# Kernel optimization log

Hardware: AMD Instinct MI355X
Metric: run time of the kernel (lower is better)

Reference implementation:

```python
import jax, jax.numpy as jnp
import numpy as np

N, E, IN, H, OUT, G = 100000, 1600000, 9, 64, 6, 1024
EPS = 1e-5


def setup_inputs() -> dict:
    key = jax.random.key(0)
    ks = jax.random.split(key, 24)
    inp = {
        "x": jax.random.normal(ks[0], (N, IN), dtype=jnp.float32),
        "edge_index": jax.random.randint(ks[1], (2, E), 0, N, dtype=jnp.int64),
        "edge_weight": jax.random.uniform(ks[2], (E,), dtype=jnp.float32),
        "batch": jnp.sort(jax.random.randint(ks[3], (N,), 0, G, dtype=jnp.int64)),
    }
    def lin(k, fan_in, fan_out):
        return jax.random.normal(k, (fan_in, fan_out), dtype=jnp.float32) / np.sqrt(fan_in)
    # GraphConv layer 0: IN -> H; layers 1,2: H -> H
    inp["W_rel0"], inp["W_root0"], inp["b0"] = lin(ks[4], IN, H), lin(ks[5], IN, H), jnp.zeros((H,), jnp.float32)
    inp["W_rel1"], inp["W_root1"], inp["b1"] = lin(ks[6], H, H), lin(ks[7], H, H), jnp.zeros((H,), jnp.float32)
    inp["W_rel2"], inp["W_root2"], inp["b2"] = lin(ks[8], H, H), lin(ks[9], H, H), jnp.zeros((H,), jnp.float32)
    # BatchNorm params for the first num_layers-1 = 2 layers
    inp["g0"], inp["be0"] = jnp.ones((H,), jnp.float32), jnp.zeros((H,), jnp.float32)
    inp["g1"], inp["be1"] = jnp.ones((H,), jnp.float32), jnp.zeros((H,), jnp.float32)
    # MLP head
    inp["W_l1"], inp["b_l1"] = lin(ks[10], H, H), jnp.zeros((H,), jnp.float32)
    inp["W_l2"], inp["b_l2"] = lin(ks[11], H, OUT), jnp.zeros((OUT,), jnp.float32)
    return inp


def graph_conv(x, src, dst, ew, W_rel, W_root, b):
    # PyG GraphConv: out = aggr_add(e_ji * x_j) @ W_rel + b + x @ W_root
    msg = x[src] * ew[:, None]                      # [E, F] gather
    agg = jax.ops.segment_sum(msg, dst, num_segments=x.shape[0])  # [N, F] scatter-add
    return agg @ W_rel + b + x @ W_root


def batch_norm(x, g, b):
    m = jnp.mean(x, axis=0)
    v = jnp.var(x, axis=0)
    return (x - m) * jax.lax.rsqrt(v + EPS) * g + b


def reference(x, edge_index, edge_weight, batch,
              W_rel0, W_root0, b0, W_rel1, W_root1, b1, W_rel2, W_root2, b2,
              g0, be0, g1, be1, W_l1, b_l1, W_l2, b_l2):
    src, dst = edge_index[0], edge_index[1]
    # layer 0: conv -> BN -> relu (dropout p applied only in training; eval here)
    h = graph_conv(x, src, dst, edge_weight, W_rel0, W_root0, b0)
    h = jax.nn.relu(batch_norm(h, g0, be0))
    # layer 1
    h = graph_conv(h, src, dst, edge_weight, W_rel1, W_root1, b1)
    h = jax.nn.relu(batch_norm(h, g1, be1))
    # layer 2 (no norm/relu)
    h = graph_conv(h, src, dst, edge_weight, W_rel2, W_root2, b2)
    # global mean pool over graphs
    summed = jax.ops.segment_sum(h, batch, num_segments=G)            # [G, H]
    counts = jax.ops.segment_sum(jnp.ones((h.shape[0],), h.dtype), batch, num_segments=G)
    pooled = summed / jnp.maximum(counts, 1.0)[:, None]
    # MLP head
    z = jax.nn.relu(pooled @ W_l1 + b_l1)
    return z @ W_l2 + b_l2
```

## Files before the change

kernel.cpp:

```cpp
#include <hip/hip_runtime.h>
#include <hip/hip_fp16.h>

constexpr int N    = 100000;
constexpr int E    = 1600000;
constexpr int FIN  = 9;
constexpr int OUTF = 6;
constexpr int G    = 1024;
constexpr int NPB  = 256;
constexpr int NB   = (N + NPB - 1) / NPB;
constexpr int CH   = 2048;
constexpr int NCH  = (E + CH - 1) / CH;
constexpr int BCAP = 4864;
constexpr int CBCAP= BCAP + NPB + 8;
constexpr int EBUF = 5888;
constexpr int ZCNT = 256 + G * 64;

typedef _Float16 f16x8 __attribute__((ext_vector_type(8)));
typedef float    f32x4 __attribute__((ext_vector_type(4)));

__device__ __forceinline__ void atomAddF(float* p, float v) { unsafeAtomicAdd(p, v); }

__global__ __launch_bounds__(256) void initK(int* __restrict__ cursor, float* __restrict__ zeros,
    const float* __restrict__ x, __half* __restrict__ x9)
{
    int i = blockIdx.x * 256 + threadIdx.x;
    if (i < NB) cursor[i] = i * BCAP;
    if (i < ZCNT) zeros[i] = 0.f;
    if (i < N * FIN) x9[i] = __float2half(x[i]);
}

__global__ __launch_bounds__(256) void passA(const int* __restrict__ src, const int* __restrict__ dst,
    const float* __restrict__ ew, int* __restrict__ cursor, int2* __restrict__ bucketed)
{
    __shared__ int h[NB];
    __shared__ int hb[NB];
    int t = threadIdx.x;
    for (int i = t; i < NB; i += 256) h[i] = 0;
    __syncthreads();
    int base = blockIdx.x * CH;
    int myS[8], myD[8], rk[8]; float myW[8];
#pragma unroll
    for (int i = 0; i < 8; i++) {
        int e = base + i * 256 + t;
        if (e < E) {
            myS[i] = src[e]; myD[i] = dst[e]; myW[i] = ew[e];
            rk[i] = atomicAdd(&h[myD[i] >> 8], 1);
        } else myD[i] = -1;
    }
    __syncthreads();
    for (int i = t; i < NB; i += 256) hb[i] = h[i] ? atomicAdd(&cursor[i], h[i]) : 0;
    __syncthreads();
#pragma unroll
    for (int i = 0; i < 8; i++) if (myD[i] >= 0) {
        int packed = myS[i] | ((myD[i] & 255) << 24);
        bucketed[hb[myD[i] >> 8] + rk[i]] = make_int2(packed, __float_as_int(myW[i]));
    }
}

__global__ __launch_bounds__(NPB) void passB(const int* __restrict__ cursor,
    const int2* __restrict__ bucketed, int* __restrict__ ebeg, int* __restrict__ eend,
    int2* __restrict__ csr)
{
    __shared__ int2 ebuf[EBUF];
    __shared__ int cl[NPB], sa[NPB], sb[NPB], curs[NPB];
    int b = blockIdx.x, t = threadIdx.x;
    int node0 = b * NPB;
    int nnode = min(NPB, N - node0);
    int cnt = cursor[b] - b * BCAP;
    int abase = b * BCAP;
    int base = b * CBCAP;
    bool fits = (cnt <= EBUF);
    cl[t] = 0;
    __syncthreads();
    for (int e = t; e < cnt; e += NPB) {
        int2 r = bucketed[abase + e];
        if (fits) ebuf[e] = r;
        atomicAdd(&cl[((unsigned)r.x) >> 24], 1);
    }
    __syncthreads();
    int deg = cl[t];
    int pc = (deg + 1) & ~1;
    int* cur = sa; int* nxt = sb;
    cur[t] = pc;
    __syncthreads();
    for (int o = 1; o < NPB; o <<= 1) {
        int v = cur[t];
        if (t >= o) v += cur[t - o];
        nxt[t] = v;
        __syncthreads();
        int* tmp = cur; cur = nxt; nxt = tmp;
    }
    int off = cur[t] - pc;
    if (t < nnode) { ebeg[node0 + t] = base + off; eend[node0 + t] = base + off + deg; }
    curs[t] = off;
    __syncthreads();
    for (int e = t; e < cnt; e += NPB) {
        int2 r = fits ? ebuf[e] : bucketed[abase + e];
        int dl = ((unsigned)r.x) >> 24;
        int pos = base + atomicAdd(&curs[dl], 1);
        csr[pos] = make_int2(r.x & 0x00FFFFFF, r.y);
    }
    __syncthreads();
    if (t < nnode && (deg & 1)) csr[base + off + deg] = make_int2(0, 0);
    if (t < 4) csr[base + cur[NPB - 1] + t] = make_int2(0, 0);
}

__global__ __launch_bounds__(256) void wprep(const float* __restrict__ Wrel1, const float* __restrict__ Wroot1,
    const float* __restrict__ Wrel2, const float* __restrict__ Wroot2, __half* __restrict__ Wt)
{
    int i = blockIdx.x * 256 + threadIdx.x;
    int layer = i >> 13, r = i & 8191;
    int c = r >> 6, k = r & 63;
    const float* Wrel = layer ? Wrel2 : Wrel1;
    const float* Wroot = layer ? Wroot2 : Wroot1;
    float v = (c < 64) ? Wrel[k * 64 + c] : Wroot[k * 64 + (c - 64)];
    Wt[i] = __float2half(v);
}

__global__ __launch_bounds__(256) void gather9(const __half* __restrict__ x9,
    const int2* __restrict__ csr, const int* __restrict__ ebeg, const int* __restrict__ eend,
    float* __restrict__ agg9)
{
    int t = threadIdx.x, lane = t & 63;
    int es = lane >> 4, fc = min(lane & 15, FIN - 1);
    int wv = (blockIdx.x * blockDim.x + t) >> 6;
    int nw = (gridDim.x * blockDim.x) >> 6;
    for (int n = wv; n < N; n += nw) {
        int beg = ebeg[n], end = eend[n];
        int last = end - 1;
        int2 eA0 = csr[min(beg + es,      last)];
        int2 eB0 = csr[min(beg + 4 + es,  last)];
        int2 eA1 = csr[min(beg + 8 + es,  last)];
        int2 eB1 = csr[min(beg + 12 + es, last)];
        __half xA = x9[(size_t)eA0.x * FIN + fc];
        __half xB = x9[(size_t)eB0.x * FIN + fc];
        float a0 = 0.f, a1 = 0.f;
        for (int k = beg; k < end; k += 8) {
            int2 eA2 = csr[min(k + 16 + es, last)];
            int2 eB2 = csr[min(k + 20 + es, last)];
            __half nxA = x9[(size_t)eA1.x * FIN + fc];
            __half nxB = x9[(size_t)eB1.x * FIN + fc];
            float wA = (k + es     < end) ? __int_as_float(eA0.y) : 0.f;
            float wB = (k + 4 + es < end) ? __int_as_float(eB0.y) : 0.f;
            a0 = fmaf(wA, __half2float(xA), a0);
            a1 = fmaf(wB, __half2float(xB), a1);
            eA0 = eA1; eB0 = eB1; eA1 = eA2; eB1 = eB2;
            xA = nxA; xB = nxB;
        }
        float r = a0 + a1;
        r += __shfl(r, lane ^ 16, 64);
        r += __shfl(r, lane ^ 32, 64);
        if (lane < FIN) agg9[(size_t)n * FIN + lane] = r;
    }
}

__global__ __launch_bounds__(256) void proj0post(const float* __restrict__ x,
    const float* __restrict__ agg9, const float* __restrict__ Wrel,
    const float* __restrict__ Wroot, const float* __restrict__ bias,
    __half* __restrict__ H0, float* __restrict__ stats)
{
    int t = threadIdx.x, j = t & 63;
    int nl = __builtin_amdgcn_readfirstlane(t >> 6);
    float wrel[FIN], wroot[FIN];
#pragma unroll
    for (int k = 0; k < FIN; k++) { wrel[k] = Wrel[k * 64 + j]; wroot[k] = Wroot[k * 64 + j]; }
    float bj = bias[j];
    float s1 = 0.f, s2 = 0.f;
    const int ntiles = N / 4;
    for (int tile = blockIdx.x; tile < ntiles; tile += gridDim.x) {
        int n = tile * 4 + nl;
        const float* xr = x + (size_t)n * FIN;
        const float* ar = agg9 + (size_t)n * FIN;
        float acc = bj;
#pragma unroll
        for (int k = 0; k < FIN; k++) {
            acc = fmaf(ar[k], wrel[k], acc);
            acc = fmaf(xr[k], wroot[k], acc);
        }
        H0[(size_t)n * 64 + j] = __float2half(acc);
        s1 += acc; s2 += acc * acc;
    }
    __shared__ float sred[256];
    sred[t] = s1; __syncthreads();
    if (t < 64) atomAddF(&stats[t], sred[t] + sred[t+64] + sred[t+128] + sred[t+192]);
    __syncthreads();
    sred[t] = s2; __syncthreads();
    if (t < 64) atomAddF(&stats[64 + t], sred[t] + sred[t+64] + sred[t+128] + sred[t+192]);
}

__global__ __launch_bounds__(256) void projm(const __half* __restrict__ Hin, const __half* __restrict__ Wt,
    const float* __restrict__ bias, const float* __restrict__ stats,
    const float* __restrict__ gam, const float* __restrict__ bet,
    __half* __restrict__ P, __half* __restrict__ Hout)
{
    int t = threadIdx.x, lane = t & 63;
    int wv = blockIdx.x * 4 + (t >> 6);
    int nw = gridDim.x * 4;
    int n16 = lane & 15, quad = lane >> 4;
    constexpr float invN = 1.0f / (float)N;
    float sc[16], sh[16];
#pragma unroll
    for (int jj = 0; jj < 16; jj++) {
        int k = (jj < 8) ? (quad * 8 + jj) : (32 + quad * 8 + (jj - 8));
        float m = stats[k] * invN;
        float v = stats[64 + k] * invN - m * m;
        sc[jj] = gam[k] * rsqrtf(v + 1e-5f);
        sh[jj] = bet[k] - m * sc[jj];
    }
    f16x8 bf[8][2];
#pragma unroll
    for (int ct = 0; ct < 8; ct++)
#pragma unroll
        for (int kh = 0; kh < 2; kh++)
            bf[ct][kh] = *(const f16x8*)(Wt + (size_t)(ct * 16 + n16) * 64 + kh * 32 + quad * 8);
    float bcol[4];
#pragma unroll
    for (int i = 0; i < 4; i++) bcol[i] = bias[i * 16 + n16];
    const int NT = N / 16;
    for (int tile = wv; tile < NT; tile += nw) {
        int n0 = tile * 16;
        f16x8 r0 = *(const f16x8*)(Hin + (size_t)(n0 + n16) * 64 + quad * 8);
        f16x8 r1 = *(const f16x8*)(Hin + (size_t)(n0 + n16) * 64 + 32 + quad * 8);
        f16x8 a0, a1;
#pragma unroll
        for (int jj = 0; jj < 8; jj++) {
            a0[jj] = (_Float16)fmaxf(fmaf((float)r0[jj], sc[jj],     sh[jj]),     0.f);
            a1[jj] = (_Float16)fmaxf(fmaf((float)r1[jj], sc[jj + 8], sh[jj + 8]), 0.f);
        }
        f32x4 acc[8];
#pragma unroll
        for (int ct = 0; ct < 8; ct++) {
            f32x4 c = {0.f, 0.f, 0.f, 0.f};
            c = __builtin_amdgcn_mfma_f32_16x16x32_f16(a0, bf[ct][0], c, 0, 0, 0);
            c = __builtin_amdgcn_mfma_f32_16x16x32_f16(a1, bf[ct][1], c, 0, 0, 0);
            acc[ct] = c;
        }
#pragma unroll
        for (int ct = 0; ct < 8; ct++) {
#pragma unroll
            for (int r = 0; r < 4; r++) {
                int n = n0 + quad * 4 + r;
                if (ct < 4) P[(size_t)n * 64 + ct * 16 + n16] = __float2half(acc[ct][r]);
                else Hout[(size_t)n * 64 + (ct - 4) * 16 + n16] = __float2half(acc[ct][r] + bcol[ct - 4]);
            }
        }
    }
}

template<int EPI>
__global__ __launch_bounds__(256) void gather(const __half* __restrict__ P, __half* H,
    const int2* __restrict__ csr, const int* __restrict__ ebeg, const int* __restrict__ eend,
    float* __restrict__ stats, const int* __restrict__ batch, float* __restrict__ pool)
{
    int t = threadIdx.x, lane = t & 63;
    int wv = (blockIdx.x * blockDim.x + t) >> 6;
    int nw = (gridDim.x * blockDim.x) >> 6;
    float s1 = 0.f, s2 = 0.f;
    const int NPAIR = N / 2;
    for (int pr = wv; pr < NPAIR; pr += nw) {
        int n0 = 2 * pr, n1 = n0 + 1;
        int b0 = ebeg[n0], m0 = (eend[n0] - b0 + 1) >> 1;
        int b1 = ebeg[n1], m1 = (eend[n1] - b1 + 1) >> 1;
        const int4* q0 = (const int4*)csr + (b0 >> 1);
        const int4* q1 = (const int4*)csr + (b1 >> 1);
        int c0 = max(m0 - 1, 0), c1 = max(m1 - 1, 0);
        float x0 = __half2float(H[(size_t)n0 * 64 + lane]);
        float x1 = __half2float(H[(size_t)n1 * 64 + lane]);
        int4 qaA = q0[0],           qbA = q0[min(1, c0)];
        int4 qcA = q1[0],           qdA = q1[min(1, c1)];
        int4 qaB = q0[min(2, c0)],  qbB = q0[min(3, c0)];
        int4 qcB = q1[min(2, c1)],  qdB = q1[min(3, c1)];
        __half pa0 = P[(size_t)qaA.x * 64 + lane], pa1 = P[(size_t)qaA.z * 64 + lane];
        __half pb0 = P[(size_t)qbA.x * 64 + lane], pb1 = P[(size_t)qbA.z * 64 + lane];
        __half pc0 = P[(size_t)qcA.x * 64 + lane], pc1 = P[(size_t)qcA.z * 64 + lane];
        __half pd0 = P[(size_t)qdA.x * 64 + lane], pd1 = P[(size_t)qdA.z * 64 + lane];
        float a0 = 0.f, a1 = 0.f, a2 = 0.f, a3 = 0.f;
        float a4 = 0.f, a5 = 0.f, a6 = 0.f, a7 = 0.f;
        int mm = max(m0, m1);
        for (int k = 0; k < mm; k += 2) {
            int4 qaC = q0[min(k + 4, c0)], qbC = q0[min(k + 5, c0)];
            int4 qcC = q1[min(k + 4, c1)], qdC = q1[min(k + 5, c1)];
            __half na0 = P[(size_t)qaB.x * 64 + lane], na1 = P[(size_t)qaB.z * 64 + lane];
            __half nb0 = P[(size_t)qbB.x * 64 + lane], nb1 = P[(size_t)qbB.z * 64 + lane];
            __half nc0 = P[(size_t)qcB.x * 64 + lane], nc1 = P[(size_t)qcB.z * 64 + lane];
            __half nd0 = P[(size_t)qdB.x * 64 + lane], nd1 = P[(size_t)qdB.z * 64 + lane];
            float wa = (k     < m0) ? __int_as_float(qaA.y) : 0.f;
            float wA = (k     < m0) ? __int_as_float(qaA.w) : 0.f;
            float wb = (k + 1 < m0) ? __int_as_float(qbA.y) : 0.f;
            float wB = (k + 1 < m0) ? __int_as_float(qbA.w) : 0.f;
            float wc = (k     < m1) ? __int_as_float(qcA.y) : 0.f;
            float wC = (k     < m1) ? __int_as_float(qcA.w) : 0.f;
            float wd = (k + 1 < m1) ? __int_as_float(qdA.y) : 0.f;
            float wD = (k + 1 < m1) ? __int_as_float(qdA.w) : 0.f;
            a0 = fmaf(wa, __half2float(pa0), a0); a1 = fmaf(wA, __half2float(pa1), a1);
            a2 = fmaf(wb, __half2float(pb0), a2); a3 = fmaf(wB, __half2float(pb1), a3);
            a4 = fmaf(wc, __half2float(pc0), a4); a5 = fmaf(wC, __half2float(pc1), a5);
            a6 = fmaf(wd, __half2float(pd0), a6); a7 = fmaf(wD, __half2float(pd1), a7);
            qaA = qaB; qbA = qbB; qcA = qcB; qdA = qdB;
            qaB = qaC; qbB = qbC; qcB = qcC; qdB = qdC;
            pa0 = na0; pa1 = na1; pb0 = nb0; pb1 = nb1;
            pc0 = nc0; pc1 = nc1; pd0 = nd0; pd1 = nd1;
        }
        float r0 = x0 + ((a0 + a2) + (a1 + a3));
        float r1 = x1 + ((a4 + a6) + (a5 + a7));
        if constexpr (EPI == 0) {
            H[(size_t)n0 * 64 + lane] = __float2half(r0);
            H[(size_t)n1 * 64 + lane] = __float2half(r1);
            s1 += r0 + r1; s2 += r0 * r0 + r1 * r1;
        } else {
            atomAddF(&pool[batch[n0] * 64 + lane], r0);
            atomAddF(&pool[batch[n1] * 64 + lane], r1);
        }
    }
    if constexpr (EPI == 0) {
        __shared__ float sred[256];
        sred[t] = s1; __syncthreads();
        if (t < 64) atomAddF(&stats[t], sred[t] + sred[t+64] + sred[t+128] + sred[t+192]);
        __syncthreads();
        sred[t] = s2; __syncthreads();
        if (t < 64) atomAddF(&stats[64 + t], sred[t] + sred[t+64] + sred[t+128] + sred[t+192]);
    }
}

__global__ __launch_bounds__(64) void head(const float* __restrict__ pool,
    const int* __restrict__ batch, const float* __restrict__ Wl1, const float* __restrict__ bl1,
    const float* __restrict__ Wl2, const float* __restrict__ bl2, float* __restrict__ out)
{
    int g = blockIdx.x, t = threadIdx.x;
    __shared__ float sp[64];
    __shared__ float sz[64];
    __shared__ int scnt;
    if (t == 0) {
        int lo = 0, hi = N;
        while (lo < hi) { int m = (lo + hi) >> 1; if (batch[m] < g) lo = m + 1; else hi = m; }
        int lo2 = lo, hi2 = N;
        while (lo2 < hi2) { int m = (lo2 + hi2) >> 1; if (batch[m] < g + 1) lo2 = m + 1; else hi2 = m; }
        scnt = lo2 - lo;
    }
    __syncthreads();
    float cnt = fmaxf((float)scnt, 1.0f);
    sp[t] = pool[g * 64 + t] / cnt;
    __syncthreads();
    float acc = bl1[t];
#pragma unroll
    for (int k = 0; k < 64; k++) acc = fmaf(sp[k], Wl1[k * 64 + t], acc);
    sz[t] = fmaxf(acc, 0.f);
    __syncthreads();
    if (t < OUTF) {
        float o = bl2[t];
#pragma unroll
        for (int k = 0; k < 64; k++) o = fmaf(sz[k], Wl2[k * OUTF + t], o);
        out[g * OUTF + t] = o;
    }
}

extern "C" void kernel_launch(void* const* d_in, const int* in_sizes, int n_in,
                              void* d_out, int out_size, void* d_ws, size_t ws_size,
                              hipStream_t stream)
{
    const float* x     = (const float*)d_in[0];
    const int*   ei    = (const int*)d_in[1];
    const float* ew    = (const float*)d_in[2];
    const int*   batch = (const int*)d_in[3];
    const float* Wrel0 = (const float*)d_in[4];
    const float* Wroot0= (const float*)d_in[5];
    const float* b0    = (const float*)d_in[6];
    const float* Wrel1 = (const float*)d_in[7];
    const float* Wroot1= (const float*)d_in[8];
    const float* b1    = (const float*)d_in[9];
    const float* Wrel2 = (const float*)d_in[10];
    const float* Wroot2= (const float*)d_in[11];
    const float* b2    = (const float*)d_in[12];
    const float* g0    = (const float*)d_in[13];
    const float* be0   = (const float*)d_in[14];
    const float* g1    = (const float*)d_in[15];
    const float* be1   = (const float*)d_in[16];
    const float* Wl1   = (const float*)d_in[17];
    const float* bl1   = (const float*)d_in[18];
    const float* Wl2   = (const float*)d_in[19];
    const float* bl2   = (const float*)d_in[20];
    const int* srcI = ei;
    const int* dstI = ei + E;

    __half* Ha     = (__half*)d_ws;
    __half* Hb     = Ha + (size_t)N * 64;
    __half* P      = Hb + (size_t)N * 64;
    int2*   csr    = (int2*)(P + (size_t)N * 64);
    int*    ebeg   = (int*)(csr + (size_t)NB * CBCAP);
    int*    eend   = ebeg + N;
    int*    cursor = eend + N;
    float*  stats0 = (float*)(cursor + NB);
    float*  stats1 = stats0 + 128;
    float*  pool   = stats1 + 128;
    __half* Wt1    = (__half*)(pool + G * 64);
    __half* Wt2    = Wt1 + 128 * 64;
    float*  agg9   = (float*)(Wt2 + 128 * 64);
    __half* x9     = (__half*)(agg9 + (size_t)N * FIN);
    int2*   bucketed = (int2*)Ha;

    initK<<<(N * FIN + 255) / 256, 256, 0, stream>>>(cursor, stats0, x, x9);
    passA<<<NCH, 256, 0, stream>>>(srcI, dstI, ew, cursor, bucketed);
    passB<<<NB, NPB, 0, stream>>>(cursor, bucketed, ebeg, eend, csr);
    wprep<<<64, 256, 0, stream>>>(Wrel1, Wroot1, Wrel2, Wroot2, Wt1);

    gather9<<<2048, 256, 0, stream>>>(x9, csr, ebeg, eend, agg9);
    proj0post<<<2048, 256, 0, stream>>>(x, agg9, Wrel0, Wroot0, b0, Ha, stats0);

    projm<<<1024, 256, 0, stream>>>(Ha, Wt1, b1, stats0, g0, be0, P, Hb);
    gather<0><<<2048, 256, 0, stream>>>(P, Hb, csr, ebeg, eend, stats1, nullptr, nullptr);

    projm<<<1024, 256, 0, stream>>>(Hb, Wt2, b2, stats1, g1, be1, P, Ha);
    gather<1><<<2048, 256, 0, stream>>>(P, Ha, csr, ebeg, eend, nullptr, batch, pool);

    head<<<G, 64, 0, stream>>>(pool, batch, Wl1, bl1, Wl2, bl2, (float*)d_out);
}
```

Baseline: 480.0 us.

## Fuse layer-0 gather with projection and deepen prefetch in gather loop

Merges the 9-feature neighbor gather with the layer-0 projection and BN-stat accumulation into one kernel. The aggregated features are broadcast by shuffle instead of written to and re-read from an agg9 buffer, which saves a launch and a global round trip. Separately, the 64-wide gather loop now prefetches one more pipeline stage of P values and edge weights, so more memory latency is in flight at the cost of extra registers. In the fused kernel each lane loads the x row directly, which may produce redundant uncoalesced reads.

```diff
diff --git a/kernel.cpp b/kernel.cpp
--- a/kernel.cpp
+++ b/kernel.cpp
@@ -117,12 +117,18 @@
     Wt[i] = __float2half(v);
 }
 
-__global__ __launch_bounds__(256) void gather9(const __half* __restrict__ x9,
+__global__ __launch_bounds__(256) void g9proj(const __half* __restrict__ x9,
     const int2* __restrict__ csr, const int* __restrict__ ebeg, const int* __restrict__ eend,
-    float* __restrict__ agg9)
+    const float* __restrict__ x, const float* __restrict__ Wrel, const float* __restrict__ Wroot,
+    const float* __restrict__ bias, __half* __restrict__ H0, float* __restrict__ stats)
 {
     int t = threadIdx.x, lane = t & 63;
     int es = lane >> 4, fc = min(lane & 15, FIN - 1);
+    float wrel[FIN], wroot[FIN];
+#pragma unroll
+    for (int k = 0; k < FIN; k++) { wrel[k] = Wrel[k * 64 + lane]; wroot[k] = Wroot[k * 64 + lane]; }
+    float bj = bias[lane];
+    float s1 = 0.f, s2 = 0.f;
     int wv = (blockIdx.x * blockDim.x + t) >> 6;
     int nw = (gridDim.x * blockDim.x) >> 6;
     for (int n = wv; n < N; n += nw) {
@@ -150,35 +156,15 @@
         float r = a0 + a1;
         r += __shfl(r, lane ^ 16, 64);
         r += __shfl(r, lane ^ 32, 64);
-        if (lane < FIN) agg9[(size_t)n * FIN + lane] = r;
-    }
-}
-
-__global__ __launch_bounds__(256) void proj0post(const float* __restrict__ x,
-    const float* __restrict__ agg9, const float* __restrict__ Wrel,
-    const float* __restrict__ Wroot, const float* __restrict__ bias,
-    __half* __restrict__ H0, float* __restrict__ stats)
-{
-    int t = threadIdx.x, j = t & 63;
-    int nl = __builtin_amdgcn_readfirstlane(t >> 6);
-    float wrel[FIN], wroot[FIN];
-#pragma unroll
-    for (int k = 0; k < FIN; k++) { wrel[k] = Wrel[k * 64 + j]; wroot[k] = Wroot[k * 64 + j]; }
-    float bj = bias[j];
-    float s1 = 0.f, s2 = 0.f;
-    const int ntiles = N / 4;
-    for (int tile = blockIdx.x; tile < ntiles; tile += gridDim.x) {
-        int n = tile * 4 + nl;
-        const float* xr = x + (size_t)n * FIN;
-        const float* ar = agg9 + (size_t)n * FIN;
-        float acc = bj;
-#pragma unroll
-        for (int k = 0; k < FIN; k++) {
-            acc = fmaf(ar[k], wrel[k], acc);
-            acc = fmaf(xr[k], wroot[k], acc);
-        }
-        H0[(size_t)n * 64 + j] = __float2half(acc);
-        s1 += acc; s2 += acc * acc;
+        float h = bj;
+#pragma unroll
+        for (int k2 = 0; k2 < FIN; k2++) {
+            float ak = __shfl(r, k2, 64);
+            h = fmaf(ak, wrel[k2], h);
+            h = fmaf(x[(size_t)n * FIN + k2], wroot[k2], h);
+        }
+        H0[(size_t)n * 64 + lane] = __float2half(h);
+        s1 += h; s2 += h * h;
     }
     __shared__ float sred[256];
     sred[t] = s1; __syncthreads();
@@ -266,40 +252,50 @@
         int c0 = max(m0 - 1, 0), c1 = max(m1 - 1, 0);
         float x0 = __half2float(H[(size_t)n0 * 64 + lane]);
         float x1 = __half2float(H[(size_t)n1 * 64 + lane]);
-        int4 qaA = q0[0],           qbA = q0[min(1, c0)];
-        int4 qcA = q1[0],           qdA = q1[min(1, c1)];
-        int4 qaB = q0[min(2, c0)],  qbB = q0[min(3, c0)];
-        int4 qcB = q1[min(2, c1)],  qdB = q1[min(3, c1)];
-        __half pa0 = P[(size_t)qaA.x * 64 + lane], pa1 = P[(size_t)qaA.z * 64 + lane];
-        __half pb0 = P[(size_t)qbA.x * 64 + lane], pb1 = P[(size_t)qbA.z * 64 + lane];
-        __half pc0 = P[(size_t)qcA.x * 64 + lane], pc1 = P[(size_t)qcA.z * 64 + lane];
-        __half pd0 = P[(size_t)qdA.x * 64 + lane], pd1 = P[(size_t)qdA.z * 64 + lane];
+        int mm = max(m0, m1);
+        int4 qa = q0[0], qb = q0[min(1, c0)], qc = q1[0], qd = q1[min(1, c1)];
+        __half v0a0 = P[(size_t)qa.x * 64 + lane], v0a1 = P[(size_t)qa.z * 64 + lane];
+        __half v0b0 = P[(size_t)qb.x * 64 + lane], v0b1 = P[(size_t)qb.z * 64 + lane];
+        __half v0c0 = P[(size_t)qc.x * 64 + lane], v0c1 = P[(size_t)qc.z * 64 + lane];
+        __half v0d0 = P[(size_t)qd.x * 64 + lane], v0d1 = P[(size_t)qd.z * 64 + lane];
+        float w0a = (0 < m0) ? __int_as_float(qa.y) : 0.f, w0A = (0 < m0) ? __int_as_float(qa.w) : 0.f;
+        float w0b = (1 < m0) ? __int_as_float(qb.y) : 0.f, w0B = (1 < m0) ? __int_as_float(qb.w) : 0.f;
+        float w0c = (0 < m1) ? __int_as_float(qc.y) : 0.f, w0C = (0 < m1) ? __int_as_float(qc.w) : 0.f;
+        float w0d = (1 < m1) ? __int_as_float(qd.y) : 0.f, w0D = (1 < m1) ? __int_as_float(qd.w) : 0.f;
+        qa = q0[min(2, c0)]; qb = q0[min(3, c0)]; qc = q1[min(2, c1)]; qd = q1[min(3, c1)];
+        __half v1a0 = P[(size_t)qa.x * 64 + lane], v1a1 = P[(size_t)qa.z * 64 + lane];
+        __half v1b0 = P[(size_t)qb.x * 64 + lane], v1b1 = P[(size_t)qb.z * 64 + lane];
+        __half v1c0 = P[(size_t)qc.x * 64 + lane], v1c1 = P[(size_t)qc.z * 64 + lane];
+        __half v1d0 = P[(size_t)qd.x * 64 + lane], v1d1 = P[(size_t)qd.z * 64 + lane];
+        float w1a = (2 < m0) ? __int_as_float(qa.y) : 0.f, w1A = (2 < m0) ? __int_as_float(qa.w) : 0.f;
+        float w1b = (3 < m0) ? __int_as_float(qb.y) : 0.f, w1B = (3 < m0) ? __int_as_float(qb.w) : 0.f;
+        float w1c = (2 < m1) ? __int_as_float(qc.y) : 0.f, w1C = (2 < m1) ? __int_as_float(qc.w) : 0.f;
+        float w1d = (3 < m1) ? __int_as_float(qd.y) : 0.f, w1D = (3 < m1) ? __int_as_float(qd.w) : 0.f;
+        int4 Qa = q0[min(4, c0)], Qb = q0[min(5, c0)], Qc = q1[min(4, c1)], Qd = q1[min(5, c1)];
         float a0 = 0.f, a1 = 0.f, a2 = 0.f, a3 = 0.f;
         float a4 = 0.f, a5 = 0.f, a6 = 0.f, a7 = 0.f;
-        int mm = max(m0, m1);
         for (int k = 0; k < mm; k += 2) {
-            int4 qaC = q0[min(k + 4, c0)], qbC = q0[min(k + 5, c0)];
-            int4 qcC = q1[min(k + 4, c1)], qdC = q1[min(k + 5, c1)];
-            __half na0 = P[(size_t)qaB.x * 64 + lane], na1 = P[(size_t)qaB.z * 64 + lane];
-            __half nb0 = P[(size_t)qbB.x * 64 + lane], nb1 = P[(size_t)qbB.z * 64 + lane];
-            __half nc0 = P[(size_t)qcB.x * 64 + lane], nc1 = P[(size_t)qcB.z * 64 + lane];
-            __half nd0 = P[(size_t)qdB.x * 64 + lane], nd1 = P[(size_t)qdB.z * 64 + lane];
-            float wa = (k     < m0) ? __int_as_float(qaA.y) : 0.f;
-            float wA = (k     < m0) ? __int_as_float(qaA.w) : 0.f;
-            float wb = (k + 1 < m0) ? __int_as_float(qbA.y) : 0.f;
-            float wB = (k + 1 < m0) ? __int_as_float(qbA.w) : 0.f;
-            float wc = (k     < m1) ? __int_as_float(qcA.y) : 0.f;
-            float wC = (k     < m1) ? __int_as_float(qcA.w) : 0.f;
-            float wd = (k + 1 < m1) ? __int_as_float(qdA.y) : 0.f;
-            float wD = (k + 1 < m1) ? __int_as_float(qdA.w) : 0.f;
-            a0 = fmaf(wa, __half2float(pa0), a0); a1 = fmaf(wA, __half2float(pa1), a1);
-            a2 = fmaf(wb, __half2float(pb0), a2); a3 = fmaf(wB, __half2float(pb1), a3);
-            a4 = fmaf(wc, __half2float(pc0), a4); a5 = fmaf(wC, __half2float(pc1), a5);
-            a6 = fmaf(wd, __half2float(pd0), a6); a7 = fmaf(wD, __half2float(pd1), a7);
-            qaA = qaB; qbA = qbB; qcA = qcB; qdA = qdB;
-            qaB = qaC; qbB = qbC; qcB = qcC; qdB = qdC;
-            pa0 = na0; pa1 = na1; pb0 = nb0; pb1 = nb1;
-            pc0 = nc0; pc1 = nc1; pd0 = nd0; pd1 = nd1;
+            int4 Na = q0[min(k + 6, c0)], Nb = q0[min(k + 7, c0)];
+            int4 Nc = q1[min(k + 6, c1)], Nd = q1[min(k + 7, c1)];
+            __half v2a0 = P[(size_t)Qa.x * 64 + lane], v2a1 = P[(size_t)Qa.z * 64 + lane];
+            __half v2b0 = P[(size_t)Qb.x * 64 + lane], v2b1 = P[(size_t)Qb.z * 64 + lane];
+            __half v2c0 = P[(size_t)Qc.x * 64 + lane], v2c1 = P[(size_t)Qc.z * 64 + lane];
+            __half v2d0 = P[(size_t)Qd.x * 64 + lane], v2d1 = P[(size_t)Qd.z * 64 + lane];
+            float w2a = (k + 4 < m0) ? __int_as_float(Qa.y) : 0.f, w2A = (k + 4 < m0) ? __int_as_float(Qa.w) : 0.f;
+            float w2b = (k + 5 < m0) ? __int_as_float(Qb.y) : 0.f, w2B = (k + 5 < m0) ? __int_as_float(Qb.w) : 0.f;
+            float w2c = (k + 4 < m1) ? __int_as_float(Qc.y) : 0.f, w2C = (k + 4 < m1) ? __int_as_float(Qc.w) : 0.f;
+            float w2d = (k + 5 < m1) ? __int_as_float(Qd.y) : 0.f, w2D = (k + 5 < m1) ? __int_as_float(Qd.w) : 0.f;
+            a0 = fmaf(w0a, __half2float(v0a0), a0); a1 = fmaf(w0A, __half2float(v0a1), a1);
+            a2 = fmaf(w0b, __half2float(v0b0), a2); a3 = fmaf(w0B, __half2float(v0b1), a3);
+            a4 = fmaf(w0c, __half2float(v0c0), a4); a5 = fmaf(w0C, __half2float(v0c1), a5);
+            a6 = fmaf(w0d, __half2float(v0d0), a6); a7 = fmaf(w0D, __half2float(v0d1), a7);
+            w0a = w1a; w0A = w1A; w0b = w1b; w0B = w1B; w0c = w1c; w0C = w1C; w0d = w1d; w0D = w1D;
+            w1a = w2a; w1A = w2A; w1b = w2b; w1B = w2B; w1c = w2c; w1C = w2C; w1d = w2d; w1D = w2D;
+            v0a0 = v1a0; v0a1 = v1a1; v0b0 = v1b0; v0b1 = v1b1;
+            v0c0 = v1c0; v0c1 = v1c1; v0d0 = v1d0; v0d1 = v1d1;
+            v1a0 = v2a0; v1a1 = v2a1; v1b0 = v2b0; v1b1 = v2b1;
+            v1c0 = v2c0; v1c1 = v2c1; v1d0 = v2d0; v1d1 = v2d1;
+            Qa = Na; Qb = Nb; Qc = Nc; Qd = Nd;
         }
         float r0 = x0 + ((a0 + a2) + (a1 + a3));
         float r1 = x1 + ((a4 + a6) + (a5 + a7));
@@ -394,8 +390,7 @@
     float*  pool   = stats1 + 128;
     __half* Wt1    = (__half*)(pool + G * 64);
     __half* Wt2    = Wt1 + 128 * 64;
-    float*  agg9   = (float*)(Wt2 + 128 * 64);
-    __half* x9     = (__half*)(agg9 + (size_t)N * FIN);
+    __half* x9     = Wt2 + 128 * 64;
     int2*   bucketed = (int2*)Ha;
 
     initK<<<(N * FIN + 255) / 256, 256, 0, stream>>>(cursor, stats0, x, x9);
@@ -403,8 +398,7 @@
     passB<<<NB, NPB, 0, stream>>>(cursor, bucketed, ebeg, eend, csr);
     wprep<<<64, 256, 0, stream>>>(Wrel1, Wroot1, Wrel2, Wroot2, Wt1);
 
-    gather9<<<2048, 256, 0, stream>>>(x9, csr, ebeg, eend, agg9);
-    proj0post<<<2048, 256, 0, stream>>>(x, agg9, Wrel0, Wroot0, b0, Ha, stats0);
+    g9proj<<<2048, 256, 0, stream>>>(x9, csr, ebeg, eend, x, Wrel0, Wroot0, b0, Ha, stats0);
 
     projm<<<1024, 256, 0, stream>>>(Ha, Wt1, b1, stats0, g0, be0, P, Hb);
     gather<0><<<2048, 256, 0, stream>>>(P, Hb, csr, ebeg, eend, stats1, nullptr, nullptr);
```

Result: no change. 485.3 us (+1.1%).
